# Optimization experiments

Measured on AMD Instinct MI355X. Metric: run time of the kernel, lower is better.

## Reference

```python
import jax, jax.numpy as jnp
import numpy as np

N_NODES = 100_000
N_EDGES = 3_200_000
NR = 10_000
NRHO = 10_000
CUTOFF = 6.0
RHO_MAX = 60.0


def natural_cubic_coeffs(x, y):
    """Natural cubic spline coefficients. x:[K], y:[K,C] -> a,b,c,d each [K-1,C]."""
    K, C = y.shape
    h = np.diff(x)
    rhs = 6.0 * ((y[2:] - y[1:-1]) / h[1:, None] - (y[1:-1] - y[:-2]) / h[:-1, None])
    n = K - 2
    diag = 2.0 * (h[:-1] + h[1:])
    off = h[1:-1]
    # Thomas algorithm for the tridiagonal system (natural BC: M[0]=M[K-1]=0)
    cp = np.zeros(n)
    dp = np.zeros((n, C))
    cp[0] = off[0] / diag[0] if n > 1 else 0.0
    dp[0] = rhs[0] / diag[0]
    for i in range(1, n):
        denom = diag[i] - off[i - 1] * cp[i - 1]
        if i < n - 1:
            cp[i] = off[i] / denom
        dp[i] = (rhs[i] - off[i - 1] * dp[i - 1]) / denom
    M = np.zeros((K, C))
    M[n] = dp[n - 1]
    for i in range(n - 2, -1, -1):
        M[i + 1] = dp[i] - cp[i] * M[i + 2]
    a = y[:-1]
    b = (y[1:] - y[:-1]) / h[:, None] - h[:, None] * (2.0 * M[:-1] + M[1:]) / 6.0
    c = M[:-1] / 2.0
    d = (M[1:] - M[:-1]) / (6.0 * h[:, None])
    f32 = lambda z: jnp.asarray(z, dtype=jnp.float32)
    return f32(a), f32(b), f32(c), f32(d)


def spline_eval(x, knots, a, b, c, d):
    """Piecewise cubic eval. x:[M], knots:[K], coeffs:[K-1,C] -> [M,C]."""
    idx = jnp.clip(jnp.searchsorted(knots, x, side='right') - 1, 0, knots.shape[0] - 2)
    s = (x - knots[idx])[:, None]  # offset within segment
    return a[idx] + s * (b[idx] + s * (c[idx] + s * d[idx]))


def setup_inputs() -> dict:
    key = jax.random.key(0)
    k1, k2, k3 = jax.random.split(key, 3)
    # edge displacement vectors; norms ~ chi(3)*1.2, well within cutoff
    r = jax.random.normal(k1, (N_EDGES, 3), dtype=jnp.float32) * 1.2
    src = jax.random.randint(k2, (N_EDGES,), 0, N_NODES, dtype=jnp.int32)
    dst = jax.random.randint(k3, (N_EDGES,), 0, N_NODES, dtype=jnp.int32)
    # synthetic smooth setfl tables (density, r*phi, embedding)
    rs = np.linspace(0.0, CUTOFF, NR)
    rhos_g = np.linspace(0.0, RHO_MAX, NRHO)
    density = np.exp(-rs)
    rphi = 27.2 * 0.529 * np.exp(-2.0 * rs) * (1.0 + 2.0 * rs)
    embedded = -np.sqrt(rhos_g) + 0.05 * rhos_g
    rad_a, rad_b, rad_c, rad_d = natural_cubic_coeffs(rs, np.stack([density, rphi], axis=1))
    emb_a, emb_b, emb_c, emb_d = natural_cubic_coeffs(rhos_g, embedded[:, None])
    return dict(
        r=r, src=src, dst=dst, n_nodes=N_NODES,
        rs=jnp.asarray(rs, jnp.float32), rhos=jnp.asarray(rhos_g, jnp.float32),
        rad_a=rad_a, rad_b=rad_b, rad_c=rad_c, rad_d=rad_d,
        emb_a=emb_a, emb_b=emb_b, emb_c=emb_c, emb_d=emb_d,
    )


def reference(r, src, dst, n_nodes, rs, rhos, rad_a, rad_b, rad_c, rad_d,
              emb_a, emb_b, emb_c, emb_d):
    def energy(r_):
        bl = jnp.linalg.norm(r_, axis=1)                       # [E]
        rp = spline_eval(bl, rs, rad_a, rad_b, rad_c, rad_d)   # [E,2]
        rho_e = rp[:, 0]
        phi_e = rp[:, 1] / bl                                  # rphi / r
        node_rho = jax.ops.segment_sum(rho_e, dst, num_segments=n_nodes)  # [N]
        F = spline_eval(node_rho, rhos, emb_a, emb_b, emb_c, emb_d)[:, 0]
        return jnp.sum(F) + 0.5 * jnp.sum(phi_e)

    E, dEdr = jax.value_and_grad(energy)(r)
    # r_ij = x_dst - x_src  =>  F_k = sum_{src=k} dE/dr - sum_{dst=k} dE/dr
    forces = (jax.ops.segment_sum(dEdr, src, num_segments=n_nodes)
              - jax.ops.segment_sum(dEdr, dst, num_segments=n_nodes))
    return E, forces
```

## Files before the change

kernel.cpp:

```cpp
#include <hip/hip_runtime.h>
#include <math.h>


static constexpr int BLOCK_A = 512;
static constexpr int EPB     = 4096;
static constexpr int SHIFT_P = 12;
static constexpr int NPP     = 4096;
static constexpr int PMAX    = 32;
static constexpr int KR      = 8;
static constexpr int KB      = 16;

static constexpr float QSCALE   = 524288.0f;
static constexpr float QSTEP    = 1.0f / QSCALE;
static constexpr float FSCALE   = 1024.0f;
static constexpr float FSTEP    = 1.0f / FSCALE;

__device__ __forceinline__ double block_reduce_d(double v) {
    #pragma unroll
    for (int off = 32; off > 0; off >>= 1)
        v += __shfl_down(v, off, 64);
    __shared__ double smem[16];
    const int lane = threadIdx.x & 63;
    const int wave = threadIdx.x >> 6;
    if (threadIdx.x < 16) smem[threadIdx.x] = 0.0;
    __syncthreads();
    if (lane == 0) smem[wave] = v;
    __syncthreads();
    if (wave == 0) {
        v = (lane < 16) ? smem[lane] : 0.0;
        #pragma unroll
        for (int off = 8; off > 0; off >>= 1)
            v += __shfl_down(v, off, 64);
    }
    return v;
}

__device__ __forceinline__ int clamp_idx(int i, int hi) {
    return i < 0 ? 0 : (i > hi ? hi : i);
}

__device__ __forceinline__ unsigned f2bf(float f) {
    unsigned u = __float_as_uint(f);
    return (u + 0x7FFFu + ((u >> 16) & 1u)) >> 16;
}
__device__ __forceinline__ float bf2f_hi(unsigned w) { return __uint_as_float(w & 0xFFFF0000u); }
__device__ __forceinline__ float bf2f_lo(unsigned w) { return __uint_as_float(w << 16); }
__device__ __forceinline__ unsigned fq(float f) {
    float s = f * FSCALE;
    s = fminf(fmaxf(s, -1.0e9f), 1.0e9f);
    return (unsigned)(int)rintf(s);
}

__global__ void eam_prep(
    const float* __restrict__ rad_a, const float* __restrict__ rad_b,
    const float* __restrict__ rad_c, const float* __restrict__ rad_d,
    const float* __restrict__ ea, const float* __restrict__ eb,
    const float* __restrict__ ec, const float* __restrict__ ed,
    float4* __restrict__ pack8, float4* __restrict__ pack4,
    int nr1, int nrho1)
{
    const int i = blockIdx.x * 256 + threadIdx.x;
    if (i < nr1) {
        pack8[2*i]   = make_float4(rad_a[2*i], rad_a[2*i+1], rad_b[2*i], rad_b[2*i+1]);
        pack8[2*i+1] = make_float4(rad_c[2*i], rad_c[2*i+1], rad_d[2*i], rad_d[2*i+1]);
    }
    if (i < nrho1)
        pack4[i] = make_float4(ea[i], eb[i], ec[i], ed[i]);
}


__global__ void __launch_bounds__(BLOCK_A) eam_p1a(
    const float* __restrict__ r, const int* __restrict__ dst,
    const float4* __restrict__ pack8,
    unsigned* __restrict__ recR, int* __restrict__ gCurR, double* __restrict__ p1,
    int n_edges, float inv_h, float h, int kmax, int P, int capR)
{
    constexpr int CH = 4 * BLOCK_A;
    __shared__ int hist[PMAX], base[PMAX], cur[PMAX], gbase[PMAX];
    __shared__ int tot;
    __shared__ unsigned buf[CH];
    __shared__ unsigned char pbk[CH];
    const int tid = threadIdx.x;
    const int e0 = blockIdx.x * EPB;
    const int e1 = min(e0 + EPB, n_edges);
    double phi = 0.0;
    for (int c0 = e0; c0 < e1; c0 += CH) {
        int node[4]; float rho[4]; bool val[4];
        if (tid < P) hist[tid] = 0;
        __syncthreads();
        #pragma unroll
        for (int k = 0; k < 4; ++k) {
            const int e = c0 + k * BLOCK_A + tid;
            val[k] = e < e1;
            node[k] = 0; rho[k] = 0.0f;
            if (val[k]) {
                const float x = r[3*e], y = r[3*e+1], z = r[3*e+2];
                const float bl = sqrtf(x*x + y*y + z*z);
                int idx = (int)(bl * inv_h); idx = idx > kmax ? kmax : idx;
                const float s = bl - (float)idx * h;
                const float4 q0 = pack8[2*idx];
                const float4 q1 = pack8[2*idx + 1];
                rho[k] = q0.x + s*(q0.z + s*(q1.x + s*q1.z));
                const float rphi = q0.y + s*(q0.w + s*(q1.y + s*q1.w));
                phi += 0.5 * (double)(rphi / bl);
                node[k] = dst[e];
                atomicAdd(&hist[node[k] >> SHIFT_P], 1);
            }
        }
        __syncthreads();
        if (tid == 0) {
            int s = 0;
            for (int i = 0; i < P; ++i) { base[i] = s; s += hist[i]; }
            tot = s;
        }
        __syncthreads();
        if (tid < P) {
            cur[tid] = base[tid];
            gbase[tid] = hist[tid] ? atomicAdd(&gCurR[tid], hist[tid]) : 0;
        }
        __syncthreads();
        #pragma unroll
        for (int k = 0; k < 4; ++k) {
            if (val[k]) {
                const int pp = node[k] >> SHIFT_P;
                int q = (int)(rho[k] * QSCALE + 0.5f);
                q = q < 0 ? 0 : (q > 0xFFFFF ? 0xFFFFF : q);
                const int pos = atomicAdd(&cur[pp], 1);
                buf[pos] = ((unsigned)(node[k] & (NPP - 1)) << 20) | (unsigned)q;
                pbk[pos] = (unsigned char)pp;
            }
        }
        __syncthreads();
        const int T = tot;
        for (int i = tid; i < T; i += BLOCK_A) {
            const int pp = pbk[i];
            const int gi = gbase[pp] + (i - base[pp]);
            if (gi < capR) recR[(size_t)pp * capR + gi] = buf[i];
        }
        __syncthreads();
    }
    const double bs = block_reduce_d(phi);
    if (tid == 0) p1[blockIdx.x] = bs;
}

__global__ void __launch_bounds__(512) eam_p1b(
    const unsigned* __restrict__ recR, const int* __restrict__ gCurR,
    float* __restrict__ partR, int capR)
{
    __shared__ unsigned acc[NPP];
    const int tid = threadIdx.x;
    const int p = blockIdx.x / KR, j = blockIdx.x % KR;
    for (int i = tid; i < NPP; i += 512) acc[i] = 0u;
    __syncthreads();
    int cnt = gCurR[p]; cnt = cnt > capR ? capR : cnt;
    const int per = (((cnt + KR - 1) / KR) + 3) & ~3;
    const int lo = j * per, hi = min(lo + per, cnt);
    const unsigned* seg = recR + (size_t)p * capR;
    int i = lo + 4 * tid;
    for (; i + 4 * 512 + 3 < hi; i += 2 * 4 * 512) {
        const uint4 a = *(const uint4*)(seg + i);
        const uint4 b = *(const uint4*)(seg + i + 4 * 512);
        atomicAdd(&acc[a.x >> 20], a.x & 0xFFFFFu);
        atomicAdd(&acc[a.y >> 20], a.y & 0xFFFFFu);
        atomicAdd(&acc[a.z >> 20], a.z & 0xFFFFFu);
        atomicAdd(&acc[a.w >> 20], a.w & 0xFFFFFu);
        atomicAdd(&acc[b.x >> 20], b.x & 0xFFFFFu);
        atomicAdd(&acc[b.y >> 20], b.y & 0xFFFFFu);
        atomicAdd(&acc[b.z >> 20], b.z & 0xFFFFFu);
        atomicAdd(&acc[b.w >> 20], b.w & 0xFFFFFu);
    }
    for (; i + 3 < hi; i += 4 * 512) {
        const uint4 a = *(const uint4*)(seg + i);
        atomicAdd(&acc[a.x >> 20], a.x & 0xFFFFFu);
        atomicAdd(&acc[a.y >> 20], a.y & 0xFFFFFu);
        atomicAdd(&acc[a.z >> 20], a.z & 0xFFFFFu);
        atomicAdd(&acc[a.w >> 20], a.w & 0xFFFFFu);
    }
    for (int t = (hi & ~3) + tid; t < hi; t += 512) {
        const unsigned w = seg[t];
        atomicAdd(&acc[w >> 20], w & 0xFFFFFu);
    }
    __syncthreads();
    float* out = partR + (size_t)blockIdx.x * NPP;
    for (int k = tid; k < NPP; k += 512) out[k] = (float)acc[k] * QSTEP;
}

__global__ void __launch_bounds__(1024) eam_p1c(
    const float* __restrict__ partR, const float4* __restrict__ pack4,
    float* __restrict__ Fp, double* __restrict__ p2,
    int n_nodes, float inv_h, float h, int kmax)
{
    const int n = blockIdx.x * 1024 + threadIdx.x;
    double fsum = 0.0;
    if (n < n_nodes) {
        const int p = n >> SHIFT_P, l = n & (NPP - 1);
        float rho = 0.0f;
        #pragma unroll
        for (int j = 0; j < KR; ++j)
            rho += partR[(size_t)(p * KR + j) * NPP + l];
        int idx = clamp_idx((int)(rho * inv_h), kmax);
        const float s = rho - (float)idx * h;
        const float4 q = pack4[idx];
        fsum = (double)(q.x + s*(q.y + s*(q.z + s*q.w)));
        Fp[n] = q.y + s*(2.0f*q.z + 3.0f*q.w*s);
    }
    const double bs = block_reduce_d(fsum);
    if (threadIdx.x == 0) p2[blockIdx.x] = bs;
}


__global__ void __launch_bounds__(BLOCK_A) eam_p3a(
    const float* __restrict__ r, const int* __restrict__ src, const int* __restrict__ dst,
    const float4* __restrict__ pack8, const float* __restrict__ Fp,
    int2* __restrict__ recF, int* __restrict__ gCurF,
    int n_edges, float inv_h, float h, int kmax, int P, int capF)
{
    constexpr int CH = 2 * BLOCK_A;
    __shared__ int hist[PMAX], base[PMAX], cur[PMAX], gbase[PMAX];
    __shared__ int tot;
    __shared__ int2 buf[2 * CH];
    __shared__ unsigned char pbk[2 * CH];
    const int tid = threadIdx.x;
    const int e0 = blockIdx.x * EPB;
    const int e1 = min(e0 + EPB, n_edges);
    for (int c0 = e0; c0 < e1; c0 += CH) {
        int si[2], di[2]; float fx[2], fy[2], fz[2]; bool val[2];
        if (tid < P) hist[tid] = 0;
        __syncthreads();
        #pragma unroll
        for (int k = 0; k < 2; ++k) {
            const int e = c0 + k * BLOCK_A + tid;
            val[k] = e < e1;
            si[k] = 0; di[k] = 0; fx[k] = fy[k] = fz[k] = 0.0f;
            if (val[k]) {
                const float x = r[3*e], y = r[3*e+1], z = r[3*e+2];
                const float bl = sqrtf(x*x + y*y + z*z);
                int idx = (int)(bl * inv_h); idx = idx > kmax ? kmax : idx;
                const float s = bl - (float)idx * h;
                const float4 q0 = pack8[2*idx];
                const float4 q1 = pack8[2*idx + 1];
                const float drho  = q0.z + s*(2.0f*q1.x + 3.0f*q1.z*s);
                const float rphi  = q0.y + s*(q0.w + s*(q1.y + s*q1.w));
                const float drphi = q0.w + s*(2.0f*q1.y + 3.0f*q1.w*s);
                const float inv_bl = 1.0f / bl;
                const float dphi = (drphi - rphi * inv_bl) * inv_bl;
                si[k] = src[e]; di[k] = dst[e];
                const float g = Fp[di[k]] * drho + 0.5f * dphi;
                const float coef = g * inv_bl;
                fx[k] = coef * x; fy[k] = coef * y; fz[k] = coef * z;
                atomicAdd(&hist[si[k] >> SHIFT_P], 1);
                atomicAdd(&hist[di[k] >> SHIFT_P], 1);
            }
        }
        __syncthreads();
        if (tid == 0) {
            int s = 0;
            for (int i = 0; i < P; ++i) { base[i] = s; s += hist[i]; }
            tot = s;
        }
        __syncthreads();
        if (tid < P) {
            cur[tid] = base[tid];
            gbase[tid] = hist[tid] ? atomicAdd(&gCurF[tid], hist[tid]) : 0;
        }
        __syncthreads();
        #pragma unroll
        for (int k = 0; k < 2; ++k) {
            if (val[k]) {
                {
                    const int pp = si[k] >> SHIFT_P;
                    const int pos = atomicAdd(&cur[pp], 1);
                    buf[pos] = make_int2(
                        (int)(((unsigned)(si[k] & (NPP-1)) << 16) | f2bf(fx[k])),
                        (int)((f2bf(fy[k]) << 16) | f2bf(fz[k])));
                    pbk[pos] = (unsigned char)pp;
                }
                {
                    const int pp = di[k] >> SHIFT_P;
                    const int pos = atomicAdd(&cur[pp], 1);
                    buf[pos] = make_int2(
                        (int)(((unsigned)(di[k] & (NPP-1)) << 16) | f2bf(-fx[k])),
                        (int)((f2bf(-fy[k]) << 16) | f2bf(-fz[k])));
                    pbk[pos] = (unsigned char)pp;
                }
            }
        }
        __syncthreads();
        const int T = tot;
        for (int i = tid; i < T; i += BLOCK_A) {
            const int pp = pbk[i];
            const int gi = gbase[pp] + (i - base[pp]);
            if (gi < capF) recF[(size_t)pp * capF + gi] = buf[i];
        }
        __syncthreads();
    }
}

__global__ void __launch_bounds__(512) eam_p3b(
    const int2* __restrict__ recF, const int* __restrict__ gCurF,
    int* __restrict__ partF, int capF)
{
    __shared__ unsigned acc[NPP * 3];
    const int tid = threadIdx.x;
    const int p = blockIdx.x / KB, j = blockIdx.x % KB;
    for (int i = tid; i < NPP * 3; i += 512) acc[i] = 0u;
    __syncthreads();
    int cnt = gCurF[p]; cnt = cnt > capF ? capF : cnt;
    const int per = (((cnt + KB - 1) / KB) + 3) & ~3;
    const int lo = j * per, hi = min(lo + per, cnt);
    const int2* seg = recF + (size_t)p * capF;
    int i = lo + 2 * tid;
    for (; i + 6 * 512 + 1 < hi; i += 8 * 512) {
        const uint4 a = *(const uint4*)(seg + i);
        const uint4 b = *(const uint4*)(seg + i + 2 * 512);
        const uint4 c = *(const uint4*)(seg + i + 4 * 512);
        const uint4 d = *(const uint4*)(seg + i + 6 * 512);
        int li;
        li = (int)(a.x >> 16) * 3;
        atomicAdd(&acc[li+0], fq(bf2f_lo(a.x))); atomicAdd(&acc[li+1], fq(bf2f_hi(a.y))); atomicAdd(&acc[li+2], fq(bf2f_lo(a.y)));
        li = (int)(a.z >> 16) * 3;
        atomicAdd(&acc[li+0], fq(bf2f_lo(a.z))); atomicAdd(&acc[li+1], fq(bf2f_hi(a.w))); atomicAdd(&acc[li+2], fq(bf2f_lo(a.w)));
        li = (int)(b.x >> 16) * 3;
        atomicAdd(&acc[li+0], fq(bf2f_lo(b.x))); atomicAdd(&acc[li+1], fq(bf2f_hi(b.y))); atomicAdd(&acc[li+2], fq(bf2f_lo(b.y)));
        li = (int)(b.z >> 16) * 3;
        atomicAdd(&acc[li+0], fq(bf2f_lo(b.z))); atomicAdd(&acc[li+1], fq(bf2f_hi(b.w))); atomicAdd(&acc[li+2], fq(bf2f_lo(b.w)));
        li = (int)(c.x >> 16) * 3;
        atomicAdd(&acc[li+0], fq(bf2f_lo(c.x))); atomicAdd(&acc[li+1], fq(bf2f_hi(c.y))); atomicAdd(&acc[li+2], fq(bf2f_lo(c.y)));
        li = (int)(c.z >> 16) * 3;
        atomicAdd(&acc[li+0], fq(bf2f_lo(c.z))); atomicAdd(&acc[li+1], fq(bf2f_hi(c.w))); atomicAdd(&acc[li+2], fq(bf2f_lo(c.w)));
        li = (int)(d.x >> 16) * 3;
        atomicAdd(&acc[li+0], fq(bf2f_lo(d.x))); atomicAdd(&acc[li+1], fq(bf2f_hi(d.y))); atomicAdd(&acc[li+2], fq(bf2f_lo(d.y)));
        li = (int)(d.z >> 16) * 3;
        atomicAdd(&acc[li+0], fq(bf2f_lo(d.z))); atomicAdd(&acc[li+1], fq(bf2f_hi(d.w))); atomicAdd(&acc[li+2], fq(bf2f_lo(d.w)));
    }
    for (; i + 1 < hi; i += 2 * 512) {
        const uint4 a = *(const uint4*)(seg + i);
        int li = (int)(a.x >> 16) * 3;
        atomicAdd(&acc[li+0], fq(bf2f_lo(a.x))); atomicAdd(&acc[li+1], fq(bf2f_hi(a.y))); atomicAdd(&acc[li+2], fq(bf2f_lo(a.y)));
        li = (int)(a.z >> 16) * 3;
        atomicAdd(&acc[li+0], fq(bf2f_lo(a.z))); atomicAdd(&acc[li+1], fq(bf2f_hi(a.w))); atomicAdd(&acc[li+2], fq(bf2f_lo(a.w)));
    }
    for (int t = (hi & ~1) + tid; t < hi; t += 512) {
        const int2 rc = seg[t];
        const unsigned w0 = (unsigned)rc.x, w1 = (unsigned)rc.y;
        const int li = (int)(w0 >> 16) * 3;
        atomicAdd(&acc[li+0], fq(bf2f_lo(w0)));
        atomicAdd(&acc[li+1], fq(bf2f_hi(w1)));
        atomicAdd(&acc[li+2], fq(bf2f_lo(w1)));
    }
    __syncthreads();
    int* out = partF + (size_t)blockIdx.x * (NPP * 3);
    for (int k = tid; k < NPP * 3; k += 512) out[k] = (int)acc[k];
}

__global__ void __launch_bounds__(1024) eam_p3c(
    const int* __restrict__ partF, float* __restrict__ outF, int n_nodes)
{
    const int g = blockIdx.x * 1024 + threadIdx.x;
    if (g >= 3 * n_nodes) return;
    const int n = g / 3, c = g - 3 * n;
    const int p = n >> SHIFT_P, l = n & (NPP - 1);
    int v = 0;
    #pragma unroll
    for (int j = 0; j < KB; ++j)
        v += partF[(size_t)(p * KB + j) * (NPP * 3) + l * 3 + c];
    outF[g] = (float)v * FSTEP;
}

__global__ void __launch_bounds__(256) eam_final_e(
    const double* __restrict__ p1, int n1,
    const double* __restrict__ p2, int n2,
    float* __restrict__ outE)
{
    double v = 0.0;
    for (int i = threadIdx.x; i < n1; i += 256) v += p1[i];
    for (int i = threadIdx.x; i < n2; i += 256) v += p2[i];
    const double bs = block_reduce_d(v);
    if (threadIdx.x == 0) *outE = (float)bs;
}


__global__ void __launch_bounds__(256) eam_pass1(
    const float* __restrict__ r, const int* __restrict__ dst,
    const float* __restrict__ rs,
    const float* __restrict__ rad_a, const float* __restrict__ rad_b,
    const float* __restrict__ rad_c, const float* __restrict__ rad_d,
    float* __restrict__ node_rho, double* __restrict__ p1,
    int n_edges, float inv_h, int kmax)
{
    const int e = blockIdx.x * 256 + threadIdx.x;
    double phi_half = 0.0;
    if (e < n_edges) {
        const float x = r[3*e], y = r[3*e+1], z = r[3*e+2];
        const float bl = sqrtf(x*x + y*y + z*z);
        const int idx = clamp_idx((int)(bl * inv_h), kmax);
        const float s = bl - rs[idx];
        const float a0 = rad_a[2*idx], a1 = rad_a[2*idx+1];
        const float b0 = rad_b[2*idx], b1 = rad_b[2*idx+1];
        const float c0 = rad_c[2*idx], c1 = rad_c[2*idx+1];
        const float d0 = rad_d[2*idx], d1 = rad_d[2*idx+1];
        const float rho  = a0 + s*(b0 + s*(c0 + s*d0));
        const float rphi = a1 + s*(b1 + s*(c1 + s*d1));
        unsafeAtomicAdd(&node_rho[dst[e]], rho);
        phi_half = 0.5 * (double)(rphi / bl);
    }
    const double bs = block_reduce_d(phi_half);
    if (threadIdx.x == 0) p1[blockIdx.x] = bs;
}

__global__ void __launch_bounds__(256) eam_pass2(
    const float* __restrict__ node_rho, const float* __restrict__ rhos,
    const float* __restrict__ ea, const float* __restrict__ eb,
    const float* __restrict__ ec, const float* __restrict__ ed,
    float* __restrict__ Fp, double* __restrict__ p2,
    int n_nodes, float inv_h, int kmax)
{
    const int n = blockIdx.x * 256 + threadIdx.x;
    double fsum = 0.0;
    if (n < n_nodes) {
        const float rho = node_rho[n];
        const int idx = clamp_idx((int)(rho * inv_h), kmax);
        const float s = rho - rhos[idx];
        const float A = ea[idx], B = eb[idx], C = ec[idx], D = ed[idx];
        fsum = (double)(A + s*(B + s*(C + s*D)));
        Fp[n] = B + s*(2.0f*C + 3.0f*D*s);
    }
    const double bs = block_reduce_d(fsum);
    if (threadIdx.x == 0) p2[blockIdx.x] = bs;
}

__global__ void __launch_bounds__(256) eam_pass3(
    const float* __restrict__ r, const int* __restrict__ src,
    const int* __restrict__ dst, const float* __restrict__ rs,
    const float* __restrict__ rad_a, const float* __restrict__ rad_b,
    const float* __restrict__ rad_c, const float* __restrict__ rad_d,
    const float* __restrict__ Fp, float* __restrict__ forces,
    int n_edges, float inv_h, int kmax)
{
    const int e = blockIdx.x * 256 + threadIdx.x;
    if (e >= n_edges) return;
    const float x = r[3*e], y = r[3*e+1], z = r[3*e+2];
    const float bl = sqrtf(x*x + y*y + z*z);
    const int idx = clamp_idx((int)(bl * inv_h), kmax);
    const float s = bl - rs[idx];
    const float a1 = rad_a[2*idx+1];
    const float b0 = rad_b[2*idx], b1 = rad_b[2*idx+1];
    const float c0 = rad_c[2*idx], c1 = rad_c[2*idx+1];
    const float d0 = rad_d[2*idx], d1 = rad_d[2*idx+1];
    const float drho  = b0 + s*(2.0f*c0 + 3.0f*d0*s);
    const float rphi  = a1 + s*(b1 + s*(c1 + s*d1));
    const float drphi = b1 + s*(2.0f*c1 + 3.0f*d1*s);
    const float inv_bl = 1.0f / bl;
    const float dphi = (drphi - rphi*inv_bl) * inv_bl;
    const int si = src[e], di = dst[e];
    const float g = Fp[di]*drho + 0.5f*dphi;
    const float coef = g * inv_bl;
    const float fx = coef*x, fy = coef*y, fz = coef*z;
    unsafeAtomicAdd(&forces[3*si+0], fx);
    unsafeAtomicAdd(&forces[3*si+1], fy);
    unsafeAtomicAdd(&forces[3*si+2], fz);
    unsafeAtomicAdd(&forces[3*di+0], -fx);
    unsafeAtomicAdd(&forces[3*di+1], -fy);
    unsafeAtomicAdd(&forces[3*di+2], -fz);
}


extern "C" void kernel_launch(void* const* d_in, const int* in_sizes, int n_in,
                              void* d_out, int out_size, void* d_ws, size_t ws_size,
                              hipStream_t stream) {
    const float* r     = (const float*)d_in[0];
    const int*   src   = (const int*)d_in[1];
    const int*   dst   = (const int*)d_in[2];
    const float* rs    = (const float*)d_in[4];
    const float* rhos  = (const float*)d_in[5];
    const float* rad_a = (const float*)d_in[6];
    const float* rad_b = (const float*)d_in[7];
    const float* rad_c = (const float*)d_in[8];
    const float* rad_d = (const float*)d_in[9];
    const float* ea    = (const float*)d_in[10];
    const float* eb    = (const float*)d_in[11];
    const float* ec    = (const float*)d_in[12];
    const float* ed    = (const float*)d_in[13];

    const int n_edges = in_sizes[0] / 3;
    const int n_nodes = (out_size - 1) / 3;
    const int nr      = in_sizes[4];
    const int nrho    = in_sizes[5];

    float* outE = (float*)d_out;
    float* outF = (float*)d_out + 1;

    const float inv_hr   = (float)((double)(nr - 1) / 6.0);
    const float hr       = (float)(6.0 / (double)(nr - 1));
    const float inv_hrho = (float)((double)(nrho - 1) / 60.0);
    const float hrho     = (float)(60.0 / (double)(nrho - 1));

    auto al = [](size_t x) { return (x + 255) & ~(size_t)255; };
    char* ws = (char*)d_ws;

    const int P    = (n_nodes + NPP - 1) >> SHIFT_P;
    const int nbA  = (n_edges + EPB - 1) / EPB;
    const int nb1c = (n_nodes + 1023) / 1024;
    const int nb3c = (3 * n_nodes + 1023) / 1024;
    const int capR = (n_edges / P + n_edges / (8 * P) + 2048) & ~3;
    const int capF = (2 * n_edges / P + n_edges / (4 * P) + 4096) & ~3;

    size_t off = 0;
    float4*   pack8 = (float4*)(ws + off);   off += al((size_t)(nr - 1) * 32);
    float4*   pack4 = (float4*)(ws + off);   off += al((size_t)(nrho - 1) * 16);
    int*      gCur  = (int*)(ws + off);      off += al((size_t)2 * PMAX * 4);
    float*    Fp    = (float*)(ws + off);    off += al((size_t)n_nodes * 4);
    double*   p1b   = (double*)(ws + off);   off += al((size_t)nbA * 8);
    double*   p2b   = (double*)(ws + off);   off += al((size_t)nb1c * 8);
    float*    partR = (float*)(ws + off);    off += al((size_t)P * KR * NPP * 4);
    int*      partF = (int*)(ws + off);      off += al((size_t)P * KB * NPP * 12);
    unsigned* recR  = (unsigned*)(ws + off); off += al((size_t)P * capR * 4);
    int2*     recF  = (int2*)(ws + off);     off += al((size_t)P * capF * 8);
    const size_t need = off;

    if (P <= PMAX && ws_size >= need) {
        int* gCurR = gCur;
        int* gCurF = gCur + PMAX;
        hipMemsetAsync(gCur, 0, (size_t)2 * PMAX * 4, stream);
        const int npk = (nr - 1) > (nrho - 1) ? (nr - 1) : (nrho - 1);
        eam_prep<<<(npk + 255) / 256, 256, 0, stream>>>(
            rad_a, rad_b, rad_c, rad_d, ea, eb, ec, ed, pack8, pack4, nr - 1, nrho - 1);
        eam_p1a<<<nbA, BLOCK_A, 0, stream>>>(
            r, dst, pack8, recR, gCurR, p1b, n_edges, inv_hr, hr, nr - 2, P, capR);
        eam_p1b<<<P * KR, 512, 0, stream>>>(recR, gCurR, partR, capR);
        eam_p1c<<<nb1c, 1024, 0, stream>>>(
            partR, pack4, Fp, p2b, n_nodes, inv_hrho, hrho, nrho - 2);
        eam_p3a<<<nbA, BLOCK_A, 0, stream>>>(
            r, src, dst, pack8, Fp, recF, gCurF, n_edges, inv_hr, hr, nr - 2, P, capF);
        eam_p3b<<<P * KB, 512, 0, stream>>>(recF, gCurF, partF, capF);
        eam_p3c<<<nb3c, 1024, 0, stream>>>(partF, outF, n_nodes);
        eam_final_e<<<1, 256, 0, stream>>>(p1b, nbA, p2b, nb1c, outE);
    } else {
        size_t o = 0;
        float* node_rho = (float*)(ws + o); o += al((size_t)n_nodes * 4);
        float* Fp2      = (float*)(ws + o); o += al((size_t)n_nodes * 4);
        const int nb_e = (n_edges + 255) / 256;
        const int nb_n = (n_nodes + 255) / 256;
        double* p1 = (double*)(ws + o); o += al((size_t)nb_e * 8);
        double* p2 = (double*)(ws + o);
        hipMemsetAsync(d_out, 0, (size_t)out_size * sizeof(float), stream);
        hipMemsetAsync(node_rho, 0, (size_t)n_nodes * sizeof(float), stream);
        eam_pass1<<<nb_e, 256, 0, stream>>>(r, dst, rs, rad_a, rad_b, rad_c, rad_d,
                                            node_rho, p1, n_edges, inv_hr, nr - 2);
        eam_pass2<<<nb_n, 256, 0, stream>>>(node_rho, rhos, ea, eb, ec, ed,
                                            Fp2, p2, n_nodes, inv_hrho, nrho - 2);
        eam_final_e<<<1, 256, 0, stream>>>(p1, nb_e, p2, nb_n, outE);
        eam_pass3<<<nb_e, 256, 0, stream>>>(r, src, dst, rs, rad_a, rad_b, rad_c, rad_d,
                                            Fp2, outF, n_edges, inv_hr, nr - 2);
    }
}
```

Before: 252.6 us.

## Process one chunk per block in binning kernels with wave-parallel prefix scan

The two edge-binning kernels now have each block handle a single chunk (4096 edges in pass 1, 2048 in pass 3) instead of looping over several smaller chunks. Each thread keeps more records in registers, and a wave-level shuffle scan replaces the serial single-thread prefix sum over partitions. The separate memset of the global counters is folded into the prep kernel. The aim is fewer barriers and serial steps and fewer launches, in exchange for more blocks, more global atomics on the partition counters, and higher register use.

New measurement: 236.4 us. 1.07x faster.

```diff
diff --git a/kernel.cpp b/kernel.cpp
--- a/kernel.cpp
+++ b/kernel.cpp
@@ -2,18 +2,18 @@
 #include <math.h>
 
 
-static constexpr int BLOCK_A = 512;
-static constexpr int EPB     = 4096;
 static constexpr int SHIFT_P = 12;
 static constexpr int NPP     = 4096;
 static constexpr int PMAX    = 32;
 static constexpr int KR      = 8;
 static constexpr int KB      = 16;
-
-static constexpr float QSCALE   = 524288.0f;
-static constexpr float QSTEP    = 1.0f / QSCALE;
-static constexpr float FSCALE   = 1024.0f;
-static constexpr float FSTEP    = 1.0f / FSCALE;
+static constexpr int CH1     = 4096;
+static constexpr int CH3     = 2048;
+
+static constexpr float QSCALE = 524288.0f;
+static constexpr float QSTEP  = 1.0f / QSCALE;
+static constexpr float FSCALE = 1024.0f;
+static constexpr float FSTEP  = 1.0f / FSCALE;
 
 __device__ __forceinline__ double block_reduce_d(double v) {
     #pragma unroll
@@ -57,9 +57,10 @@
     const float* __restrict__ ea, const float* __restrict__ eb,
     const float* __restrict__ ec, const float* __restrict__ ed,
     float4* __restrict__ pack8, float4* __restrict__ pack4,
-    int nr1, int nrho1)
+    int* __restrict__ gCur, int nr1, int nrho1)
 {
     const int i = blockIdx.x * 256 + threadIdx.x;
+    if (blockIdx.x == 0 && threadIdx.x < 2 * PMAX) gCur[threadIdx.x] = 0;
     if (i < nr1) {
         pack8[2*i]   = make_float4(rad_a[2*i], rad_a[2*i+1], rad_b[2*i], rad_b[2*i+1]);
         pack8[2*i+1] = make_float4(rad_c[2*i], rad_c[2*i+1], rad_d[2*i], rad_d[2*i+1]);
@@ -69,75 +70,78 @@
 }
 
 
-__global__ void __launch_bounds__(BLOCK_A) eam_p1a(
+__global__ void __launch_bounds__(512) eam_p1a(
     const float* __restrict__ r, const int* __restrict__ dst,
     const float4* __restrict__ pack8,
     unsigned* __restrict__ recR, int* __restrict__ gCurR, double* __restrict__ p1,
     int n_edges, float inv_h, float h, int kmax, int P, int capR)
 {
-    constexpr int CH = 4 * BLOCK_A;
     __shared__ int hist[PMAX], base[PMAX], cur[PMAX], gbase[PMAX];
     __shared__ int tot;
-    __shared__ unsigned buf[CH];
-    __shared__ unsigned char pbk[CH];
+    __shared__ unsigned buf[CH1];
+    __shared__ unsigned char pbk[CH1];
     const int tid = threadIdx.x;
-    const int e0 = blockIdx.x * EPB;
-    const int e1 = min(e0 + EPB, n_edges);
+    const int e0 = blockIdx.x * CH1;
+    const int e1 = min(e0 + CH1, n_edges);
     double phi = 0.0;
-    for (int c0 = e0; c0 < e1; c0 += CH) {
-        int node[4]; float rho[4]; bool val[4];
-        if (tid < P) hist[tid] = 0;
-        __syncthreads();
+    unsigned rec[8]; int pk[8]; bool val[8];
+    if (tid < P) hist[tid] = 0;
+    __syncthreads();
+    #pragma unroll
+    for (int k = 0; k < 8; ++k) {
+        const int e = e0 + k * 512 + tid;
+        val[k] = e < e1;
+        rec[k] = 0; pk[k] = 0;
+        if (val[k]) {
+            const float x = r[3*e], y = r[3*e+1], z = r[3*e+2];
+            const float bl = sqrtf(x*x + y*y + z*z);
+            int idx = (int)(bl * inv_h); idx = idx > kmax ? kmax : idx;
+            const float s = bl - (float)idx * h;
+            const float4 q0 = pack8[2*idx];
+            const float4 q1 = pack8[2*idx + 1];
+            const float rho  = q0.x + s*(q0.z + s*(q1.x + s*q1.z));
+            const float rphi = q0.y + s*(q0.w + s*(q1.y + s*q1.w));
+            phi += 0.5 * (double)(rphi / bl);
+            const int node = dst[e];
+            pk[k] = node >> SHIFT_P;
+            int q = (int)(rho * QSCALE + 0.5f);
+            q = q < 0 ? 0 : (q > 0xFFFFF ? 0xFFFFF : q);
+            rec[k] = ((unsigned)(node & (NPP - 1)) << 20) | (unsigned)q;
+            atomicAdd(&hist[pk[k]], 1);
+        }
+    }
+    __syncthreads();
+    if (tid < 64) {
+        const int lane = tid;
+        const int hv = (lane < P) ? hist[lane] : 0;
+        int s = hv;
         #pragma unroll
-        for (int k = 0; k < 4; ++k) {
-            const int e = c0 + k * BLOCK_A + tid;
-            val[k] = e < e1;
-            node[k] = 0; rho[k] = 0.0f;
-            if (val[k]) {
-                const float x = r[3*e], y = r[3*e+1], z = r[3*e+2];
-                const float bl = sqrtf(x*x + y*y + z*z);
-                int idx = (int)(bl * inv_h); idx = idx > kmax ? kmax : idx;
-                const float s = bl - (float)idx * h;
-                const float4 q0 = pack8[2*idx];
-                const float4 q1 = pack8[2*idx + 1];
-                rho[k] = q0.x + s*(q0.z + s*(q1.x + s*q1.z));
-                const float rphi = q0.y + s*(q0.w + s*(q1.y + s*q1.w));
-                phi += 0.5 * (double)(rphi / bl);
-                node[k] = dst[e];
-                atomicAdd(&hist[node[k] >> SHIFT_P], 1);
-            }
-        }
-        __syncthreads();
-        if (tid == 0) {
-            int s = 0;
-            for (int i = 0; i < P; ++i) { base[i] = s; s += hist[i]; }
-            tot = s;
-        }
-        __syncthreads();
-        if (tid < P) {
-            cur[tid] = base[tid];
-            gbase[tid] = hist[tid] ? atomicAdd(&gCurR[tid], hist[tid]) : 0;
-        }
-        __syncthreads();
-        #pragma unroll
-        for (int k = 0; k < 4; ++k) {
-            if (val[k]) {
-                const int pp = node[k] >> SHIFT_P;
-                int q = (int)(rho[k] * QSCALE + 0.5f);
-                q = q < 0 ? 0 : (q > 0xFFFFF ? 0xFFFFF : q);
-                const int pos = atomicAdd(&cur[pp], 1);
-                buf[pos] = ((unsigned)(node[k] & (NPP - 1)) << 20) | (unsigned)q;
-                pbk[pos] = (unsigned char)pp;
-            }
-        }
-        __syncthreads();
-        const int T = tot;
-        for (int i = tid; i < T; i += BLOCK_A) {
-            const int pp = pbk[i];
-            const int gi = gbase[pp] + (i - base[pp]);
-            if (gi < capR) recR[(size_t)pp * capR + gi] = buf[i];
-        }
-        __syncthreads();
+        for (int off = 1; off < 32; off <<= 1) {
+            const int t = __shfl_up(s, off, 64);
+            if (lane >= off) s += t;
+        }
+        if (lane < P) {
+            base[lane] = s - hv;
+            cur[lane]  = s - hv;
+            gbase[lane] = hv ? atomicAdd(&gCurR[lane], hv) : 0;
+        }
+        if (lane == P - 1) tot = s;
+    }
+    __syncthreads();
+    #pragma unroll
+    for (int k = 0; k < 8; ++k) {
+        if (val[k]) {
+            const int pos = atomicAdd(&cur[pk[k]], 1);
+            buf[pos] = rec[k];
+            pbk[pos] = (unsigned char)pk[k];
+        }
+    }
+    __syncthreads();
+    const int T = tot;
+    for (int i = tid; i < T; i += 512) {
+        const int pp = pbk[i];
+        const int gi = gbase[pp] + (i - base[pp]);
+        if (gi < capR) recR[(size_t)pp * capR + gi] = buf[i];
     }
     const double bs = block_reduce_d(phi);
     if (tid == 0) p1[blockIdx.x] = bs;
@@ -209,90 +213,89 @@
 }
 
 
-__global__ void __launch_bounds__(BLOCK_A) eam_p3a(
+__global__ void __launch_bounds__(512) eam_p3a(
     const float* __restrict__ r, const int* __restrict__ src, const int* __restrict__ dst,
     const float4* __restrict__ pack8, const float* __restrict__ Fp,
     int2* __restrict__ recF, int* __restrict__ gCurF,
     int n_edges, float inv_h, float h, int kmax, int P, int capF)
 {
-    constexpr int CH = 2 * BLOCK_A;
     __shared__ int hist[PMAX], base[PMAX], cur[PMAX], gbase[PMAX];
     __shared__ int tot;
-    __shared__ int2 buf[2 * CH];
-    __shared__ unsigned char pbk[2 * CH];
+    __shared__ int2 buf[2 * CH3];
+    __shared__ unsigned char pbk[2 * CH3];
     const int tid = threadIdx.x;
-    const int e0 = blockIdx.x * EPB;
-    const int e1 = min(e0 + EPB, n_edges);
-    for (int c0 = e0; c0 < e1; c0 += CH) {
-        int si[2], di[2]; float fx[2], fy[2], fz[2]; bool val[2];
-        if (tid < P) hist[tid] = 0;
-        __syncthreads();
+    const int e0 = blockIdx.x * CH3;
+    const int e1 = min(e0 + CH3, n_edges);
+    int2 sa[4], da[4]; int ps[4], pd[4]; bool val[4];
+    if (tid < P) hist[tid] = 0;
+    __syncthreads();
+    #pragma unroll
+    for (int k = 0; k < 4; ++k) {
+        const int e = e0 + k * 512 + tid;
+        val[k] = e < e1;
+        ps[k] = pd[k] = 0;
+        sa[k] = da[k] = make_int2(0, 0);
+        if (val[k]) {
+            const float x = r[3*e], y = r[3*e+1], z = r[3*e+2];
+            const float bl = sqrtf(x*x + y*y + z*z);
+            int idx = (int)(bl * inv_h); idx = idx > kmax ? kmax : idx;
+            const float s = bl - (float)idx * h;
+            const float4 q0 = pack8[2*idx];
+            const float4 q1 = pack8[2*idx + 1];
+            const float drho  = q0.z + s*(2.0f*q1.x + 3.0f*q1.z*s);
+            const float rphi  = q0.y + s*(q0.w + s*(q1.y + s*q1.w));
+            const float drphi = q0.w + s*(2.0f*q1.y + 3.0f*q1.w*s);
+            const float inv_bl = 1.0f / bl;
+            const float dphi = (drphi - rphi * inv_bl) * inv_bl;
+            const int si = src[e], di = dst[e];
+            const float g = Fp[di] * drho + 0.5f * dphi;
+            const float coef = g * inv_bl;
+            const unsigned bx = f2bf(coef * x), by = f2bf(coef * y), bz = f2bf(coef * z);
+            ps[k] = si >> SHIFT_P;
+            pd[k] = di >> SHIFT_P;
+            sa[k] = make_int2((int)(((unsigned)(si & (NPP-1)) << 16) | bx),
+                              (int)((by << 16) | bz));
+            da[k] = make_int2((int)(((unsigned)(di & (NPP-1)) << 16) | (bx ^ 0x8000u)),
+                              (int)(((by ^ 0x8000u) << 16) | (bz ^ 0x8000u)));
+            atomicAdd(&hist[ps[k]], 1);
+            atomicAdd(&hist[pd[k]], 1);
+        }
+    }
+    __syncthreads();
+    if (tid < 64) {
+        const int lane = tid;
+        const int hv = (lane < P) ? hist[lane] : 0;
+        int s = hv;
         #pragma unroll
-        for (int k = 0; k < 2; ++k) {
-            const int e = c0 + k * BLOCK_A + tid;
-            val[k] = e < e1;
-            si[k] = 0; di[k] = 0; fx[k] = fy[k] = fz[k] = 0.0f;
-            if (val[k]) {
-                const float x = r[3*e], y = r[3*e+1], z = r[3*e+2];
-                const float bl = sqrtf(x*x + y*y + z*z);
-                int idx = (int)(bl * inv_h); idx = idx > kmax ? kmax : idx;
-                const float s = bl - (float)idx * h;
-                const float4 q0 = pack8[2*idx];
-                const float4 q1 = pack8[2*idx + 1];
-                const float drho  = q0.z + s*(2.0f*q1.x + 3.0f*q1.z*s);
-                const float rphi  = q0.y + s*(q0.w + s*(q1.y + s*q1.w));
-                const float drphi = q0.w + s*(2.0f*q1.y + 3.0f*q1.w*s);
-                const float inv_bl = 1.0f / bl;
-                const float dphi = (drphi - rphi * inv_bl) * inv_bl;
-                si[k] = src[e]; di[k] = dst[e];
-                const float g = Fp[di[k]] * drho + 0.5f * dphi;
-                const float coef = g * inv_bl;
-                fx[k] = coef * x; fy[k] = coef * y; fz[k] = coef * z;
-                atomicAdd(&hist[si[k] >> SHIFT_P], 1);
-                atomicAdd(&hist[di[k] >> SHIFT_P], 1);
-            }
-        }
-        __syncthreads();
-        if (tid == 0) {
-            int s = 0;
-            for (int i = 0; i < P; ++i) { base[i] = s; s += hist[i]; }
-            tot = s;
-        }
-        __syncthreads();
-        if (tid < P) {
-            cur[tid] = base[tid];
-            gbase[tid] = hist[tid] ? atomicAdd(&gCurF[tid], hist[tid]) : 0;
-        }
-        __syncthreads();
-        #pragma unroll
-        for (int k = 0; k < 2; ++k) {
-            if (val[k]) {
-                {
-                    const int pp = si[k] >> SHIFT_P;
-                    const int pos = atomicAdd(&cur[pp], 1);
-                    buf[pos] = make_int2(
-                        (int)(((unsigned)(si[k] & (NPP-1)) << 16) | f2bf(fx[k])),
-                        (int)((f2bf(fy[k]) << 16) | f2bf(fz[k])));
-                    pbk[pos] = (unsigned char)pp;
-                }
-                {
-                    const int pp = di[k] >> SHIFT_P;
-                    const int pos = atomicAdd(&cur[pp], 1);
-                    buf[pos] = make_int2(
-                        (int)(((unsigned)(di[k] & (NPP-1)) << 16) | f2bf(-fx[k])),
-                        (int)((f2bf(-fy[k]) << 16) | f2bf(-fz[k])));
-                    pbk[pos] = (unsigned char)pp;
-                }
-            }
-        }
-        __syncthreads();
-        const int T = tot;
-        for (int i = tid; i < T; i += BLOCK_A) {
-            const int pp = pbk[i];
-            const int gi = gbase[pp] + (i - base[pp]);
-            if (gi < capF) recF[(size_t)pp * capF + gi] = buf[i];
-        }
-        __syncthreads();
+        for (int off = 1; off < 32; off <<= 1) {
+            const int t = __shfl_up(s, off, 64);
+            if (lane >= off) s += t;
+        }
+        if (lane < P) {
+            base[lane] = s - hv;
+            cur[lane]  = s - hv;
+            gbase[lane] = hv ? atomicAdd(&gCurF[lane], hv) : 0;
+        }
+        if (lane == P - 1) tot = s;
+    }
+    __syncthreads();
+    #pragma unroll
+    for (int k = 0; k < 4; ++k) {
+        if (val[k]) {
+            int pos = atomicAdd(&cur[ps[k]], 1);
+            buf[pos] = sa[k];
+            pbk[pos] = (unsigned char)ps[k];
+            pos = atomicAdd(&cur[pd[k]], 1);
+            buf[pos] = da[k];
+            pbk[pos] = (unsigned char)pd[k];
+        }
+    }
+    __syncthreads();
+    const int T = tot;
+    for (int i = tid; i < T; i += 512) {
+        const int pp = pbk[i];
+        const int gi = gbase[pp] + (i - base[pp]);
+        if (gi < capF) recF[(size_t)pp * capF + gi] = buf[i];
     }
 }
 
@@ -499,7 +502,8 @@
     char* ws = (char*)d_ws;
 
     const int P    = (n_nodes + NPP - 1) >> SHIFT_P;
-    const int nbA  = (n_edges + EPB - 1) / EPB;
+    const int nb1a = (n_edges + CH1 - 1) / CH1;
+    const int nb3a = (n_edges + CH3 - 1) / CH3;
     const int nb1c = (n_nodes + 1023) / 1024;
     const int nb3c = (3 * n_nodes + 1023) / 1024;
     const int capR = (n_edges / P + n_edges / (8 * P) + 2048) & ~3;
@@ -510,7 +514,7 @@
     float4*   pack4 = (float4*)(ws + off);   off += al((size_t)(nrho - 1) * 16);
     int*      gCur  = (int*)(ws + off);      off += al((size_t)2 * PMAX * 4);
     float*    Fp    = (float*)(ws + off);    off += al((size_t)n_nodes * 4);
-    double*   p1b   = (double*)(ws + off);   off += al((size_t)nbA * 8);
+    double*   p1b   = (double*)(ws + off);   off += al((size_t)nb1a * 8);
     double*   p2b   = (double*)(ws + off);   off += al((size_t)nb1c * 8);
     float*    partR = (float*)(ws + off);    off += al((size_t)P * KR * NPP * 4);
     int*      partF = (int*)(ws + off);      off += al((size_t)P * KB * NPP * 12);
@@ -521,20 +525,19 @@
     if (P <= PMAX && ws_size >= need) {
         int* gCurR = gCur;
         int* gCurF = gCur + PMAX;
-        hipMemsetAsync(gCur, 0, (size_t)2 * PMAX * 4, stream);
         const int npk = (nr - 1) > (nrho - 1) ? (nr - 1) : (nrho - 1);
         eam_prep<<<(npk + 255) / 256, 256, 0, stream>>>(
-            rad_a, rad_b, rad_c, rad_d, ea, eb, ec, ed, pack8, pack4, nr - 1, nrho - 1);
-        eam_p1a<<<nbA, BLOCK_A, 0, stream>>>(
+            rad_a, rad_b, rad_c, rad_d, ea, eb, ec, ed, pack8, pack4, gCur, nr - 1, nrho - 1);
+        eam_p1a<<<nb1a, 512, 0, stream>>>(
             r, dst, pack8, recR, gCurR, p1b, n_edges, inv_hr, hr, nr - 2, P, capR);
         eam_p1b<<<P * KR, 512, 0, stream>>>(recR, gCurR, partR, capR);
         eam_p1c<<<nb1c, 1024, 0, stream>>>(
             partR, pack4, Fp, p2b, n_nodes, inv_hrho, hrho, nrho - 2);
-        eam_p3a<<<nbA, BLOCK_A, 0, stream>>>(
+        eam_p3a<<<nb3a, 512, 0, stream>>>(
             r, src, dst, pack8, Fp, recF, gCurF, n_edges, inv_hr, hr, nr - 2, P, capF);
         eam_p3b<<<P * KB, 512, 0, stream>>>(recF, gCurF, partF, capF);
         eam_p3c<<<nb3c, 1024, 0, stream>>>(partF, outF, n_nodes);
-        eam_final_e<<<1, 256, 0, stream>>>(p1b, nbA, p2b, nb1c, outE);
+        eam_final_e<<<1, 256, 0, stream>>>(p1b, nb1a, p2b, nb1c, outE);
     } else {
         size_t o = 0;
         float* node_rho = (float*)(ws + o); o += al((size_t)n_nodes * 4);
```
